# Kernel tuning notes

Hardware: AMD Instinct MI355X
Metric: run time of the kernel (lower is better)

The kernel has to match this reference:

```python
import jax, jax.numpy as jnp
import numpy as np


def setup_inputs() -> dict:
    key = jax.random.key(0)
    k1, k2 = jax.random.split(key)
    B, S, E, V = 8, 512, 512, 50000
    batch = jax.random.normal(k1, (B, S, E), dtype=jnp.float32)
    emb = jax.random.normal(k2, (V, E), dtype=jnp.float32)
    return {"batch": batch, "emb": emb}


def reference(batch, emb):
    # __init__ with distance != 'L2': embedding table is L2-normalized once.
    emb_n = emb / jnp.linalg.norm(emb, axis=1, keepdims=True)  # [V, E]
    # forward: normalize batch along last (emb) dim.
    b = batch / jnp.linalg.norm(batch, axis=2, keepdims=True)  # [B, S, E]
    B, S, E = b.shape
    # cosine_distance: flatten tokens, GEMM against table, 1 - sim, argmin over V.
    mult = b.reshape(-1, E) @ emb_n.T            # [B*S, V]
    cosine_dist = 1.0 - mult
    nearest = jnp.argmin(cosine_dist, axis=1)    # [B*S]
    return nearest.reshape(B, S)
```

## Files before the change

### kernel.cpp

```cpp
#include <hip/hip_runtime.h>
#include <stdint.h>

typedef _Float16 f16;
typedef _Float16 f16x4 __attribute__((ext_vector_type(4)));
typedef _Float16 f16x8 __attribute__((ext_vector_type(8)));
typedef float    f32x4 __attribute__((ext_vector_type(4)));

__device__ __forceinline__ void llds16(const void* g, void* l) {
    __builtin_amdgcn_global_load_lds(
        (const __attribute__((address_space(1))) void*)g,
        (__attribute__((address_space(3))) void*)l, 16, 0, 0);
}

__device__ __forceinline__ unsigned long long pack_key(float s, int j) {
    unsigned u = __float_as_uint(s);
    u = (u & 0x80000000u) ? ~u : (u | 0x80000000u);
    return ((unsigned long long)u << 32) | (unsigned)(~(unsigned)j);
}

__global__ void convert_emb_kernel(const float* __restrict__ emb,
                                   f16* __restrict__ bh,
                                   float* __restrict__ rinv, int V, int E) {
    int row  = blockIdx.x * (blockDim.x >> 6) + (threadIdx.x >> 6);
    int lane = threadIdx.x & 63;
    if (row >= V) return;
    const float4* p = (const float4*)(emb + (size_t)row * E);
    int n4 = E >> 2;
    float ss = 0.f;
    for (int i = lane; i < n4; i += 64) {
        float4 v = p[i];
        ss = fmaf(v.x, v.x, ss); ss = fmaf(v.y, v.y, ss);
        ss = fmaf(v.z, v.z, ss); ss = fmaf(v.w, v.w, ss);
    }
    #pragma unroll
    for (int o = 32; o > 0; o >>= 1) ss += __shfl_down(ss, o, 64);
    if (lane == 0) rinv[row] = 1.0f / sqrtf(ss);

    for (int i = lane; i < n4; i += 64) {
        float4 v = p[i];
        f16x4 h;
        h.x = (f16)v.x; h.y = (f16)v.y; h.z = (f16)v.z; h.w = (f16)v.w;
        *(f16x4*)&bh[(size_t)row * E + i * 4] = h;
    }
}

__global__ void convert_batch_kernel(const float* __restrict__ batch,
                                     f16* __restrict__ ah, int M, int E) {
    int row  = blockIdx.x * (blockDim.x >> 6) + (threadIdx.x >> 6);
    int lane = threadIdx.x & 63;
    if (row >= M) return;
    const float4* p = (const float4*)(batch + (size_t)row * E);
    int n4 = E >> 2;
    for (int i = lane; i < n4; i += 64) {
        float4 v = p[i];
        f16x4 h;
        h.x = (f16)v.x; h.y = (f16)v.y; h.z = (f16)v.z; h.w = (f16)v.w;
        *(f16x4*)&ah[(size_t)row * E + i * 4] = h;
    }
}

__global__ void init_bmax_kernel(unsigned* __restrict__ bmax, int n) {
    int i = blockIdx.x * blockDim.x + threadIdx.x;
    for (; i < n; i += gridDim.x * blockDim.x) bmax[i] = 0u;
}

#define BM 128
#define BN 128
#define BKH 64

__global__ __launch_bounds__(256, 4) void nn_hh_kernel(
    const f16* __restrict__ Ah, const f16* __restrict__ Bh,
    const float* __restrict__ rinvP, unsigned* __restrict__ bmax,
    int M, int V, int E, int NG)
{
    __shared__ f16 sAh[BM * BKH], sBh[BM * BKH];

    const int tid  = threadIdx.x;
    const int lane = tid & 63;
    const int w    = tid >> 6;
    const int wr   = w >> 1;
    const int wc   = w & 1;
    const int fr   = lane & 15;
    const int kg   = lane >> 4;

    const int row0 = blockIdx.x * BM;
    const int col0 = blockIdx.y * BN;

    const int srow  = lane >> 3;
    const int sslot = lane & 7;
    const int xslot = sslot ^ srow;
    int aoff[4], boff[4], ldof[4];
    #pragma unroll
    for (int it = 0; it < 4; ++it) {
        int rl = w * 32 + it * 8 + srow;
        aoff[it] = (row0 + rl) * E + xslot * 8;
        int bj = col0 + rl; if (bj > V - 1) bj = V - 1;
        boff[it] = bj * E + xslot * 8;
        ldof[it] = (w * 32 + it * 8) * BKH;
    }

    f32x4 acc[4][4];
    #pragma unroll
    for (int m = 0; m < 4; ++m)
        #pragma unroll
        for (int n = 0; n < 4; ++n) acc[m][n] = (f32x4){0.f, 0.f, 0.f, 0.f};

    const int steps = E / BKH;
    for (int ks = 0; ks < steps; ++ks) {
        const int kadv = ks * BKH;
        #pragma unroll
        for (int it = 0; it < 4; ++it) {
            llds16(Ah + aoff[it] + kadv, sAh + ldof[it]);
            llds16(Bh + boff[it] + kadv, sBh + ldof[it]);
        }
        __syncthreads();

        #pragma unroll
        for (int ksub = 0; ksub < 2; ++ksub) {
            f16x8 ah[4], bh[4];
            #pragma unroll
            for (int m = 0; m < 4; ++m) {
                int row = wr * 64 + m * 16 + fr;
                int off = row * BKH + (((ksub * 4 + kg) ^ (fr & 7)) << 3);
                ah[m] = *(const f16x8*)&sAh[off];
            }
            #pragma unroll
            for (int n = 0; n < 4; ++n) {
                int col = wc * 64 + n * 16 + fr;
                int off = col * BKH + (((ksub * 4 + kg) ^ (fr & 7)) << 3);
                bh[n] = *(const f16x8*)&sBh[off];
            }
            #pragma unroll
            for (int m = 0; m < 4; ++m)
                #pragma unroll
                for (int n = 0; n < 4; ++n)
                    acc[m][n] = __builtin_amdgcn_mfma_f32_16x16x32_f16(
                        ah[m], bh[n], acc[m][n], 0, 0, 0);
        }
        __syncthreads();
    }

    const int colb = col0 + wc * 64;
    const int g    = colb >> 6;
    float ri[4];
    #pragma unroll
    for (int n = 0; n < 4; ++n) {
        int j = colb + n * 16 + fr;
        ri[n] = (j < V) ? rinvP[j] : 0.f;
    }
    #pragma unroll
    for (int m = 0; m < 4; ++m) {
        #pragma unroll
        for (int r = 0; r < 4; ++r) {
            unsigned long long best = 0ULL;
            #pragma unroll
            for (int n = 0; n < 4; ++n) {
                int j = colb + n * 16 + fr;
                if (j < V) {
                    unsigned long long key = pack_key(acc[m][n][r] * ri[n], j);
                    if (key > best) best = key;
                }
            }
            #pragma unroll
            for (int o = 8; o > 0; o >>= 1) {
                unsigned long long other = __shfl_xor(best, o, 64);
                if (other > best) best = other;
            }
            if (fr == 0 && best != 0ULL) {
                int row = row0 + wr * 64 + m * 16 + kg * 4 + r;
                atomicMax(&bmax[(size_t)row * NG + g], (unsigned)(best >> 32));
            }
        }
    }
}

#define TAU 0.008f
#define NGMAX 800

__global__ __launch_bounds__(256) void refine_kernel(
    const float* __restrict__ batch, const float* __restrict__ emb,
    const float* __restrict__ rinvP, const unsigned* __restrict__ bmax,
    int* __restrict__ out, int V, int E, int NG)
{
    const int r   = blockIdx.x;
    const int tid = threadIdx.x;
    __shared__ float arow[512];
    __shared__ float gv[NGMAX];
    __shared__ float part[4][64];
    __shared__ int   lst[NGMAX];
    __shared__ int   cnt;
    __shared__ float wmax[4];

    for (int i = tid; i < E; i += 256) arow[i] = batch[(size_t)r * E + i];
    if (tid == 0) cnt = 0;

    float lm = -3.4e38f;
    for (int g = tid; g < NG; g += 256) {
        unsigned u = bmax[(size_t)r * NG + g];
        unsigned v = (u & 0x80000000u) ? (u & 0x7FFFFFFFu) : ~u;
        float f = __uint_as_float(v);
        gv[g] = f;
        lm = fmaxf(lm, f);
    }
    #pragma unroll
    for (int o = 32; o > 0; o >>= 1) lm = fmaxf(lm, __shfl_xor(lm, o, 64));
    if ((tid & 63) == 0) wmax[tid >> 6] = lm;
    __syncthreads();
    const float m1 = fmaxf(fmaxf(wmax[0], wmax[1]), fmaxf(wmax[2], wmax[3]));
    const float thresh = m1 - TAU;

    for (int g = tid; g < NG; g += 256)
        if (gv[g] >= thresh) { int i = atomicAdd(&cnt, 1); lst[i] = g; }
    __syncthreads();
    const int n = cnt;

    const int colL = tid & 63;
    const int kq   = tid >> 6;
    unsigned long long best = 0ULL;
    for (int li = 0; li < n; ++li) {
        const int j = lst[li] * 64 + colL;
        float p = 0.f;
        if (j < V) {
            const float4* bp = (const float4*)(emb + (size_t)j * E + kq * 128);
            const float4* ap = (const float4*)(&arow[kq * 128]);
            #pragma unroll 8
            for (int i = 0; i < 32; ++i) {
                float4 b = bp[i], a = ap[i];
                p = fmaf(a.x, b.x, p); p = fmaf(a.y, b.y, p);
                p = fmaf(a.z, b.z, p); p = fmaf(a.w, b.w, p);
            }
        }
        part[kq][colL] = p;
        __syncthreads();
        if (kq == 0 && j < V) {
            float dot = (part[0][colL] + part[1][colL]) +
                        (part[2][colL] + part[3][colL]);
            unsigned long long key = pack_key(dot * rinvP[j], j);
            if (key > best) best = key;
        }
        __syncthreads();
    }

    if (tid < 64) {
        #pragma unroll
        for (int o = 32; o > 0; o >>= 1) {
            unsigned long long other = __shfl_xor(best, o, 64);
            if (other > best) best = other;
        }
        if (tid == 0) out[r] = (int)(~(unsigned)(best & 0xFFFFFFFFULL));
    }
}

__global__ void init_keys_kernel(unsigned long long* __restrict__ keys, int M) {
    int i = blockIdx.x * blockDim.x + threadIdx.x;
    if (i < M) keys[i] = 0ULL;
}

__global__ void extract_kernel(const unsigned long long* __restrict__ keys,
                               int* __restrict__ out, int M) {
    int i = blockIdx.x * blockDim.x + threadIdx.x;
    if (i < M) out[i] = (int)(~(unsigned)(keys[i] & 0xFFFFFFFFULL));
}

__global__ void inv_norms_kernel(const float* __restrict__ emb,
                                 float* __restrict__ r, int V, int E) {
    int row  = blockIdx.x * (blockDim.x >> 6) + (threadIdx.x >> 6);
    int lane = threadIdx.x & 63;
    if (row >= V) return;
    const float4* p = reinterpret_cast<const float4*>(emb + (size_t)row * E);
    float ss = 0.f;
    int n4 = E >> 2;
    for (int i = lane; i < n4; i += 64) {
        float4 v = p[i];
        ss = fmaf(v.x, v.x, ss); ss = fmaf(v.y, v.y, ss);
        ss = fmaf(v.z, v.z, ss); ss = fmaf(v.w, v.w, ss);
    }
    #pragma unroll
    for (int o = 32; o > 0; o >>= 1) ss += __shfl_down(ss, o, 64);
    if (lane == 0) r[row] = 1.0f / sqrtf(ss);
}

#define FBM 128
#define FBN 128
#define FBK 32
#define LDSPAD 4

__global__ __launch_bounds__(256) void nn_gemm_argmax(
    const float* __restrict__ batch, const float* __restrict__ emb,
    const float* __restrict__ rinv, unsigned long long* __restrict__ keys,
    int M, int V, int E)
{
    __shared__ float As[FBK][FBM + LDSPAD];
    __shared__ float Bs[FBK][FBN + LDSPAD];
    const int tid = threadIdx.x;
    const int tx  = tid & 15;
    const int ty  = tid >> 4;
    const int row0 = blockIdx.y * FBM;
    const int col0 = blockIdx.x * FBN;
    float acc[8][8];
    #pragma unroll
    for (int i = 0; i < 8; ++i)
        #pragma unroll
        for (int j = 0; j < 8; ++j) acc[i][j] = 0.f;
    const int steps = E / FBK;
    for (int ks = 0; ks < steps; ++ks) {
        const int k0 = ks * FBK;
        #pragma unroll
        for (int it = 0; it < 4; ++it) {
            int idx = it * 256 + tid;
            int rr = idx >> 3, cc = idx & 7;
            float4 v = *reinterpret_cast<const float4*>(
                &batch[(size_t)(row0 + rr) * E + k0 + cc * 4]);
            As[cc*4+0][rr] = v.x; As[cc*4+1][rr] = v.y;
            As[cc*4+2][rr] = v.z; As[cc*4+3][rr] = v.w;
        }
        #pragma unroll
        for (int it = 0; it < 4; ++it) {
            int idx = it * 256 + tid;
            int rr = idx >> 3, cc = idx & 7;
            int j = col0 + rr;
            float4 v = make_float4(0.f,0.f,0.f,0.f);
            if (j < V)
                v = *reinterpret_cast<const float4*>(&emb[(size_t)j * E + k0 + cc * 4]);
            Bs[cc*4+0][rr] = v.x; Bs[cc*4+1][rr] = v.y;
            Bs[cc*4+2][rr] = v.z; Bs[cc*4+3][rr] = v.w;
        }
        __syncthreads();
        #pragma unroll
        for (int k = 0; k < FBK; ++k) {
            float4 a0 = *reinterpret_cast<const float4*>(&As[k][ty*8]);
            float4 a1 = *reinterpret_cast<const float4*>(&As[k][ty*8+4]);
            float4 b0 = *reinterpret_cast<const float4*>(&Bs[k][tx*8]);
            float4 b1 = *reinterpret_cast<const float4*>(&Bs[k][tx*8+4]);
            float a[8] = {a0.x,a0.y,a0.z,a0.w,a1.x,a1.y,a1.z,a1.w};
            float b[8] = {b0.x,b0.y,b0.z,b0.w,b1.x,b1.y,b1.z,b1.w};
            #pragma unroll
            for (int i = 0; i < 8; ++i)
                #pragma unroll
                for (int jj = 0; jj < 8; ++jj)
                    acc[i][jj] = fmaf(a[i], b[jj], acc[i][jj]);
        }
        __syncthreads();
    }
    #pragma unroll
    for (int i = 0; i < 8; ++i) {
        const int q = row0 + ty * 8 + i;
        unsigned long long best = 0ULL;
        #pragma unroll
        for (int jj = 0; jj < 8; ++jj) {
            int j = col0 + tx * 8 + jj;
            if (j < V) {
                unsigned long long key = pack_key(acc[i][jj] * rinv[j], j);
                if (key > best) best = key;
            }
        }
        #pragma unroll
        for (int o = 8; o > 0; o >>= 1) {
            unsigned long long other = __shfl_xor(best, o, 64);
            if (other > best) best = other;
        }
        if (tx == 0 && best != 0ULL) atomicMax(&keys[q], best);
    }
}

extern "C" void kernel_launch(void* const* d_in, const int* in_sizes, int n_in,
                              void* d_out, int out_size, void* d_ws, size_t ws_size,
                              hipStream_t stream) {
    const float* batch = (const float*)d_in[0];
    const float* emb   = (const float*)d_in[1];
    int* out = (int*)d_out;

    const int M = out_size;
    const int E = in_sizes[0] / M;
    const int V = in_sizes[1] / E;
    const int NG = (V + 63) / 64;

    auto al256 = [](size_t x) { return (x + 255) & ~(size_t)255; };
    size_t o_rinv = 0;
    size_t o_keys = al256(o_rinv + (size_t)V * 4);
    size_t o_bmax = al256(o_keys + (size_t)M * 8);
    size_t o_Ah   = al256(o_bmax + (size_t)M * NG * 4);
    size_t o_Bh   = al256(o_Ah  + (size_t)M * E * 2);
    size_t need   = al256(o_Bh  + (size_t)V * E * 2);

    float* rinv = (float*)((char*)d_ws + o_rinv);
    unsigned long long* keys = (unsigned long long*)((char*)d_ws + o_keys);
    unsigned* bmax = (unsigned*)((char*)d_ws + o_bmax);

    if (ws_size >= need && E == 512 && (M % BM) == 0 && NG <= NGMAX) {
        f16* Ah = (f16*)((char*)d_ws + o_Ah);
        f16* Bh = (f16*)((char*)d_ws + o_Bh);

        convert_emb_kernel<<<(V + 3) / 4, 256, 0, stream>>>(emb, Bh, rinv, V, E);
        convert_batch_kernel<<<(M + 3) / 4, 256, 0, stream>>>(batch, Ah, M, E);
        init_bmax_kernel<<<2048, 256, 0, stream>>>(bmax, M * NG);

        dim3 grid(M / BM, (V + BN - 1) / BN);
        nn_hh_kernel<<<grid, 256, 0, stream>>>(Ah, Bh, rinv, bmax, M, V, E, NG);

        refine_kernel<<<M, 256, 0, stream>>>(batch, emb, rinv, bmax, out, V, E, NG);
    } else {
        inv_norms_kernel<<<(V + 3) / 4, 256, 0, stream>>>(emb, rinv, V, E);
        init_keys_kernel<<<(M + 255) / 256, 256, 0, stream>>>(keys, M);
        dim3 grid((V + FBN - 1) / FBN, M / FBM);
        nn_gemm_argmax<<<grid, 256, 0, stream>>>(batch, emb, rinv, keys, M, V, E);
        extract_kernel<<<(M + 255) / 256, 256, 0, stream>>>(keys, out, M);
    }
}
```

Baseline: 470.4 us.

## Double-buffer LDS in fp16 GEMM, swizzle blocks, refine at 16-column group granularity

The fp16 MFMA GEMM now double-buffers its shared-memory tiles so the next K-slice's global-to-LDS loads overlap the current MFMAs, removing one barrier per step. It also launches a 1D grid with an XCD-aware block swizzle. The per-group candidate bound shrinks from 64 to 16 columns, which means more atomics and a larger bmax array. In exchange the fp32 refine pass recomputes fewer columns per candidate group, with four groups processed per iteration. Risks are the extra atomics and bmax traffic, and possibly more candidate groups passing the threshold.

```diff
diff --git a/kernel.cpp b/kernel.cpp
--- a/kernel.cpp
+++ b/kernel.cpp
@@ -73,7 +73,7 @@
     const float* __restrict__ rinvP, unsigned* __restrict__ bmax,
     int M, int V, int E, int NG)
 {
-    __shared__ f16 sAh[BM * BKH], sBh[BM * BKH];
+    __shared__ f16 sA[2][BM * BKH], sB[2][BM * BKH];
 
     const int tid  = threadIdx.x;
     const int lane = tid & 63;
@@ -83,8 +83,14 @@
     const int fr   = lane & 15;
     const int kg   = lane >> 4;
 
-    const int row0 = blockIdx.x * BM;
-    const int col0 = blockIdx.y * BN;
+    const int nwg = gridDim.x;
+    const int bid = blockIdx.x;
+    const int swz = ((nwg & 7) == 0) ? ((bid & 7) * (nwg >> 3) + (bid >> 3)) : bid;
+    const int mblocks = M / BM;
+    const int mb = swz % mblocks;
+    const int nb = swz / mblocks;
+    const int row0 = mb * BM;
+    const int col0 = nb * BN;
 
     const int srow  = lane >> 3;
     const int sslot = lane & 7;
@@ -106,14 +112,24 @@
         for (int n = 0; n < 4; ++n) acc[m][n] = (f32x4){0.f, 0.f, 0.f, 0.f};
 
     const int steps = E / BKH;
+
+    #pragma unroll
+    for (int it = 0; it < 4; ++it) {
+        llds16(Ah + aoff[it], &sA[0][ldof[it]]);
+        llds16(Bh + boff[it], &sB[0][ldof[it]]);
+    }
+    __syncthreads();
+
     for (int ks = 0; ks < steps; ++ks) {
-        const int kadv = ks * BKH;
-        #pragma unroll
-        for (int it = 0; it < 4; ++it) {
-            llds16(Ah + aoff[it] + kadv, sAh + ldof[it]);
-            llds16(Bh + boff[it] + kadv, sBh + ldof[it]);
-        }
-        __syncthreads();
+        const int cur = ks & 1;
+        if (ks + 1 < steps) {
+            const int kadv = (ks + 1) * BKH;
+            #pragma unroll
+            for (int it = 0; it < 4; ++it) {
+                llds16(Ah + aoff[it] + kadv, &sA[cur ^ 1][ldof[it]]);
+                llds16(Bh + boff[it] + kadv, &sB[cur ^ 1][ldof[it]]);
+            }
+        }
 
         #pragma unroll
         for (int ksub = 0; ksub < 2; ++ksub) {
@@ -122,13 +138,13 @@
             for (int m = 0; m < 4; ++m) {
                 int row = wr * 64 + m * 16 + fr;
                 int off = row * BKH + (((ksub * 4 + kg) ^ (fr & 7)) << 3);
-                ah[m] = *(const f16x8*)&sAh[off];
+                ah[m] = *(const f16x8*)&sA[cur][off];
             }
             #pragma unroll
             for (int n = 0; n < 4; ++n) {
                 int col = wc * 64 + n * 16 + fr;
                 int off = col * BKH + (((ksub * 4 + kg) ^ (fr & 7)) << 3);
-                bh[n] = *(const f16x8*)&sBh[off];
+                bh[n] = *(const f16x8*)&sB[cur][off];
             }
             #pragma unroll
             for (int m = 0; m < 4; ++m)
@@ -141,7 +157,7 @@
     }
 
     const int colb = col0 + wc * 64;
-    const int g    = colb >> 6;
+    const int g0   = colb >> 4;
     float ri[4];
     #pragma unroll
     for (int n = 0; n < 4; ++n) {
@@ -152,44 +168,45 @@
     for (int m = 0; m < 4; ++m) {
         #pragma unroll
         for (int r = 0; r < 4; ++r) {
-            unsigned long long best = 0ULL;
             #pragma unroll
             for (int n = 0; n < 4; ++n) {
                 int j = colb + n * 16 + fr;
-                if (j < V) {
-                    unsigned long long key = pack_key(acc[m][n][r] * ri[n], j);
-                    if (key > best) best = key;
+                unsigned long long best =
+                    (j < V) ? pack_key(acc[m][n][r] * ri[n], j) : 0ULL;
+                #pragma unroll
+                for (int o = 8; o > 0; o >>= 1) {
+                    unsigned long long other = __shfl_xor(best, o, 64);
+                    if (other > best) best = other;
                 }
-            }
-            #pragma unroll
-            for (int o = 8; o > 0; o >>= 1) {
-                unsigned long long other = __shfl_xor(best, o, 64);
-                if (other > best) best = other;
-            }
-            if (fr == 0 && best != 0ULL) {
-                int row = row0 + wr * 64 + m * 16 + kg * 4 + r;
-                atomicMax(&bmax[(size_t)row * NG + g], (unsigned)(best >> 32));
+                if (fr == 0 && best != 0ULL) {
+                    int row = row0 + wr * 64 + m * 16 + kg * 4 + r;
+                    atomicMax(&bmax[(size_t)row * NG + g0 + n],
+                              (unsigned)(best >> 32));
+                }
             }
         }
     }
 }
 
 #define TAU 0.008f
-#define NGMAX 800
+#define NGMAX 3200
 
 __global__ __launch_bounds__(256) void refine_kernel(
     const float* __restrict__ batch, const float* __restrict__ emb,
     const float* __restrict__ rinvP, const unsigned* __restrict__ bmax,
     int* __restrict__ out, int V, int E, int NG)
 {
-    const int r   = blockIdx.x;
-    const int tid = threadIdx.x;
+    const int r    = blockIdx.x;
+    const int tid  = threadIdx.x;
+    const int lane = tid & 63;
+    const int wid  = tid >> 6;
     __shared__ float arow[512];
     __shared__ float gv[NGMAX];
-    __shared__ float part[4][64];
+    __shared__ float part[4][4][16];
     __shared__ int   lst[NGMAX];
     __shared__ int   cnt;
     __shared__ float wmax[4];
+    __shared__ unsigned long long wbest[4];
 
     for (int i = tid; i < E; i += 256) arow[i] = batch[(size_t)r * E + i];
     if (tid == 0) cnt = 0;
@@ -204,7 +221,7 @@
     }
     #pragma unroll
     for (int o = 32; o > 0; o >>= 1) lm = fmaxf(lm, __shfl_xor(lm, o, 64));
-    if ((tid & 63) == 0) wmax[tid >> 6] = lm;
+    if (lane == 0) wmax[wid] = lm;
     __syncthreads();
     const float m1 = fmaxf(fmaxf(wmax[0], wmax[1]), fmaxf(wmax[2], wmax[3]));
     const float thresh = m1 - TAU;
@@ -214,40 +231,51 @@
     __syncthreads();
     const int n = cnt;
 
-    const int colL = tid & 63;
-    const int kq   = tid >> 6;
+    const int colL = tid & 15;
+    const int kq   = (tid >> 4) & 3;
+    const int gs   = tid >> 6;
     unsigned long long best = 0ULL;
-    for (int li = 0; li < n; ++li) {
-        const int j = lst[li] * 64 + colL;
+    for (int li0 = 0; li0 < n; li0 += 4) {
+        const int li = li0 + gs;
+        int j = -1;
         float p = 0.f;
-        if (j < V) {
-            const float4* bp = (const float4*)(emb + (size_t)j * E + kq * 128);
-            const float4* ap = (const float4*)(&arow[kq * 128]);
-            #pragma unroll 8
-            for (int i = 0; i < 32; ++i) {
-                float4 b = bp[i], a = ap[i];
-                p = fmaf(a.x, b.x, p); p = fmaf(a.y, b.y, p);
-                p = fmaf(a.z, b.z, p); p = fmaf(a.w, b.w, p);
-            }
-        }
-        part[kq][colL] = p;
+        if (li < n) {
+            j = lst[li] * 16 + colL;
+            if (j < V) {
+                const float4* bp = (const float4*)(emb + (size_t)j * E + kq * 128);
+                const float4* ap = (const float4*)(&arow[kq * 128]);
+                #pragma unroll 8
+                for (int i = 0; i < 32; ++i) {
+                    float4 b = bp[i], a = ap[i];
+                    p = fmaf(a.x, b.x, p); p = fmaf(a.y, b.y, p);
+                    p = fmaf(a.z, b.z, p); p = fmaf(a.w, b.w, p);
+                }
+            }
+        }
+        part[gs][kq][colL] = p;
         __syncthreads();
-        if (kq == 0 && j < V) {
-            float dot = (part[0][colL] + part[1][colL]) +
-                        (part[2][colL] + part[3][colL]);
+        if (kq == 0 && j >= 0 && j < V) {
+            float dot = (part[gs][0][colL] + part[gs][1][colL]) +
+                        (part[gs][2][colL] + part[gs][3][colL]);
             unsigned long long key = pack_key(dot * rinvP[j], j);
             if (key > best) best = key;
         }
         __syncthreads();
     }
 
-    if (tid < 64) {
-        #pragma unroll
-        for (int o = 32; o > 0; o >>= 1) {
-            unsigned long long other = __shfl_xor(best, o, 64);
-            if (other > best) best = other;
-        }
-        if (tid == 0) out[r] = (int)(~(unsigned)(best & 0xFFFFFFFFULL));
+    #pragma unroll
+    for (int o = 32; o > 0; o >>= 1) {
+        unsigned long long other = __shfl_xor(best, o, 64);
+        if (other > best) best = other;
+    }
+    if (lane == 0) wbest[wid] = best;
+    __syncthreads();
+    if (tid == 0) {
+        unsigned long long b = wbest[0];
+        if (wbest[1] > b) b = wbest[1];
+        if (wbest[2] > b) b = wbest[2];
+        if (wbest[3] > b) b = wbest[3];
+        out[r] = (int)(~(unsigned)(b & 0xFFFFFFFFULL));
     }
 }
 
@@ -373,7 +401,7 @@
     const int M = out_size;
     const int E = in_sizes[0] / M;
     const int V = in_sizes[1] / E;
-    const int NG = (V + 63) / 64;
+    const int NG = (V + 15) / 16;
 
     auto al256 = [](size_t x) { return (x + 255) & ~(size_t)255; };
     size_t o_rinv = 0;
@@ -395,8 +423,8 @@
         convert_batch_kernel<<<(M + 3) / 4, 256, 0, stream>>>(batch, Ah, M, E);
         init_bmax_kernel<<<2048, 256, 0, stream>>>(bmax, M * NG);
 
-        dim3 grid(M / BM, (V + BN - 1) / BN);
-        nn_hh_kernel<<<grid, 256, 0, stream>>>(Ah, Bh, rinv, bmax, M, V, E, NG);
+        int nblocks = (M / BM) * ((V + BN - 1) / BN);
+        nn_hh_kernel<<<nblocks, 256, 0, stream>>>(Ah, Bh, rinv, bmax, M, V, E, NG);
 
         refine_kernel<<<M, 256, 0, stream>>>(batch, emb, rinv, bmax, out, V, E, NG);
     } else {
```

Measured after the change: 1.152 ms. 145% more time.

## Load B fragments straight from global and double-buffer A tiles in LDS

Applied to the files above, without the earlier changes.

The GEMM kernel no longer stages the embedding (B) tile through shared memory. Each lane now loads its MFMA B fragments directly from global memory, and the A tile is double-buffered so the next k-step's global-to-LDS copy overlaps the current step's MFMAs. The epilogue reduction also switches from 64-bit packed keys to a float max, packing into the sortable form only once before the atomic. The direct global B loads are 16-byte strided per row with no cross-wave reuse, so they may add memory traffic and latency.

```diff
diff --git a/kernel.cpp b/kernel.cpp
--- a/kernel.cpp
+++ b/kernel.cpp
@@ -73,7 +73,7 @@
     const float* __restrict__ rinvP, unsigned* __restrict__ bmax,
     int M, int V, int E, int NG)
 {
-    __shared__ f16 sAh[BM * BKH], sBh[BM * BKH];
+    __shared__ f16 sA[2][BM * BKH];
 
     const int tid  = threadIdx.x;
     const int lane = tid & 63;
@@ -89,16 +89,22 @@
     const int srow  = lane >> 3;
     const int sslot = lane & 7;
     const int xslot = sslot ^ srow;
-    int aoff[4], boff[4], ldof[4];
+    int aoff[4], ldof[4];
     #pragma unroll
     for (int it = 0; it < 4; ++it) {
         int rl = w * 32 + it * 8 + srow;
         aoff[it] = (row0 + rl) * E + xslot * 8;
-        int bj = col0 + rl; if (bj > V - 1) bj = V - 1;
-        boff[it] = bj * E + xslot * 8;
         ldof[it] = (w * 32 + it * 8) * BKH;
     }
 
+    const f16* bbase[4];
+    #pragma unroll
+    for (int n = 0; n < 4; ++n) {
+        int c = col0 + wc * 64 + n * 16 + fr;
+        if (c > V - 1) c = V - 1;
+        bbase[n] = Bh + (size_t)c * E + kg * 8;
+    }
+
     f32x4 acc[4][4];
     #pragma unroll
     for (int m = 0; m < 4; ++m)
@@ -106,36 +112,45 @@
         for (int n = 0; n < 4; ++n) acc[m][n] = (f32x4){0.f, 0.f, 0.f, 0.f};
 
     const int steps = E / BKH;
+
+    #pragma unroll
+    for (int it = 0; it < 4; ++it)
+        llds16(Ah + aoff[it], &sA[0][ldof[it]]);
+    __syncthreads();
+
     for (int ks = 0; ks < steps; ++ks) {
-        const int kadv = ks * BKH;
-        #pragma unroll
-        for (int it = 0; it < 4; ++it) {
-            llds16(Ah + aoff[it] + kadv, sAh + ldof[it]);
-            llds16(Bh + boff[it] + kadv, sBh + ldof[it]);
-        }
-        __syncthreads();
+        const int cur = ks & 1;
+        const int kbase = ks * BKH;
+
+        f16x8 bf[2][4];
+        #pragma unroll
+        for (int ksub = 0; ksub < 2; ++ksub)
+            #pragma unroll
+            for (int n = 0; n < 4; ++n)
+                bf[ksub][n] = *(const f16x8*)(bbase[n] + kbase + ksub * 32);
+
+        if (ks + 1 < steps) {
+            const int kadv = (ks + 1) * BKH;
+            #pragma unroll
+            for (int it = 0; it < 4; ++it)
+                llds16(Ah + aoff[it] + kadv, &sA[cur ^ 1][ldof[it]]);
+        }
 
         #pragma unroll
         for (int ksub = 0; ksub < 2; ++ksub) {
-            f16x8 ah[4], bh[4];
+            f16x8 ah[4];
             #pragma unroll
             for (int m = 0; m < 4; ++m) {
                 int row = wr * 64 + m * 16 + fr;
                 int off = row * BKH + (((ksub * 4 + kg) ^ (fr & 7)) << 3);
-                ah[m] = *(const f16x8*)&sAh[off];
-            }
-            #pragma unroll
-            for (int n = 0; n < 4; ++n) {
-                int col = wc * 64 + n * 16 + fr;
-                int off = col * BKH + (((ksub * 4 + kg) ^ (fr & 7)) << 3);
-                bh[n] = *(const f16x8*)&sBh[off];
+                ah[m] = *(const f16x8*)&sA[cur][off];
             }
             #pragma unroll
             for (int m = 0; m < 4; ++m)
                 #pragma unroll
                 for (int n = 0; n < 4; ++n)
                     acc[m][n] = __builtin_amdgcn_mfma_f32_16x16x32_f16(
-                        ah[m], bh[n], acc[m][n], 0, 0, 0);
+                        ah[m], bf[ksub][n], acc[m][n], 0, 0, 0);
         }
         __syncthreads();
     }
@@ -152,23 +167,21 @@
     for (int m = 0; m < 4; ++m) {
         #pragma unroll
         for (int r = 0; r < 4; ++r) {
-            unsigned long long best = 0ULL;
+            float best = -3.4e38f;
             #pragma unroll
             for (int n = 0; n < 4; ++n) {
                 int j = colb + n * 16 + fr;
-                if (j < V) {
-                    unsigned long long key = pack_key(acc[m][n][r] * ri[n], j);
-                    if (key > best) best = key;
-                }
+                float sc = (j < V) ? acc[m][n][r] * ri[n] : -3.4e38f;
+                best = fmaxf(best, sc);
             }
             #pragma unroll
-            for (int o = 8; o > 0; o >>= 1) {
-                unsigned long long other = __shfl_xor(best, o, 64);
-                if (other > best) best = other;
-            }
-            if (fr == 0 && best != 0ULL) {
+            for (int o = 8; o > 0; o >>= 1)
+                best = fmaxf(best, __shfl_xor(best, o, 64));
+            if (fr == 0) {
                 int row = row0 + wr * 64 + m * 16 + kg * 4 + r;
-                atomicMax(&bmax[(size_t)row * NG + g], (unsigned)(best >> 32));
+                unsigned u = __float_as_uint(best);
+                u = (u & 0x80000000u) ? ~u : (u | 0x80000000u);
+                atomicMax(&bmax[(size_t)row * NG + g], u);
             }
         }
     }
```

Result: slower. 544.7 us (+15.8%).
